# Performance work log

Hardware: AMD Instinct MI355X
Metric: run time of the kernel (lower is better)

## Reference

```python
import jax, jax.numpy as jnp
import numpy as np

N, E = 100000, 1600000
F_IN, H, K, C = 165, 128, 3, 2


def _norm_weights(edge_index, n):
    # PyG ChebConv.__norm__ with normalization='sym', lambda_max=2.0:
    # remove self loops, deg from row, w = -D^-1/2 A D^-1/2 off-diag, diag = 0.
    src, dst = edge_index[0], edge_index[1]
    mask = (src != dst).astype(jnp.float32)
    deg = jax.ops.segment_sum(mask, src, num_segments=n)
    dinv = jnp.where(deg > 0, jax.lax.rsqrt(jnp.where(deg > 0, deg, 1.0)), 0.0)
    return -dinv[src] * dinv[dst] * mask  # [E]


def _cheb_conv(x, W, b, src, dst, w, n):
    # Chebyshev recurrence: Tx0 = x, Tx1 = Lhat x, Tx_k = 2 Lhat Tx_{k-1} - Tx_{k-2}
    def prop(h):  # sparse Lhat @ h via gather + segment_sum
        return jax.ops.segment_sum(w[:, None] * h[src], dst, num_segments=n)

    out = x @ W[0]
    Tx0, Tx1 = x, prop(x)
    out = out + Tx1 @ W[1]
    for k in range(2, W.shape[0]):
        Tx2 = 2.0 * prop(Tx1) - Tx0
        out = out + Tx2 @ W[k]
        Tx0, Tx1 = Tx1, Tx2
    return out + b


def setup_inputs() -> dict:
    key = jax.random.key(0)
    ks = jax.random.split(key, 8)
    x = jax.random.normal(ks[0], (N, F_IN), dtype=jnp.float32)
    edge_index = jax.random.randint(ks[1], (2, E), 0, N, dtype=jnp.int64)
    s1 = 1.0 / np.sqrt(F_IN)
    s2 = 1.0 / np.sqrt(H)
    W1 = jax.random.uniform(ks[2], (K, F_IN, H), jnp.float32, -s1, s1)
    b1 = jnp.zeros((H,), jnp.float32)
    W2 = jax.random.uniform(ks[3], (K, H, H), jnp.float32, -s2, s2)
    b2 = jnp.zeros((H,), jnp.float32)
    Wl = jax.random.uniform(ks[4], (H, C), jnp.float32, -s2, s2)
    bl = jax.random.uniform(ks[5], (C,), jnp.float32, -s2, s2)
    return {"x": x, "edge_index": edge_index, "W1": W1, "b1": b1,
            "W2": W2, "b2": b2, "Wl": Wl, "bl": bl}


def reference(x, edge_index, W1, b1, W2, b2, Wl, bl):
    n = x.shape[0]
    src, dst = edge_index[0], edge_index[1]
    w = _norm_weights(edge_index, n)
    h = jax.nn.relu(_cheb_conv(x, W1, b1, src, dst, w, n))
    # F.dropout(training=self.training) is identity in eval mode
    h = h + _cheb_conv(h, W2, b2, src, dst, w, n)  # residual skip
    logits = jax.nn.log_softmax(h @ Wl + bl, axis=-1)
    return (logits, edge_index)
```

## Files before the change

kernel.cpp:

```cpp
#include <hip/hip_runtime.h>
#include <stdint.h>

typedef __bf16 bf16;
typedef unsigned char u8;
typedef __attribute__((ext_vector_type(8))) __bf16 bf16x8;
typedef __attribute__((ext_vector_type(4))) float f32x4;
typedef __attribute__((ext_vector_type(2))) float f32x2;

#define N_NODES 100000
#define F_IN 165
#define NB 391
#define NBLK 320

static inline int cdiv(int a, int b) { return (a + b - 1) / b; }

__device__ __forceinline__ float bfu(unsigned hw) {
  union { unsigned u; float f; } v; v.u = hw << 16; return v.f;
}
__device__ __forceinline__ unsigned packbf2(float a, float b) {
  bf16 x = (bf16)a, y = (bf16)b;
  unsigned short sx = __builtin_bit_cast(unsigned short, x);
  unsigned short sy = __builtin_bit_cast(unsigned short, y);
  return (unsigned)sx | ((unsigned)sy << 16);
}
__device__ __forceinline__ u8 f32_to_fp8(float v) {
  int t = __builtin_amdgcn_cvt_pk_fp8_f32(v, 0.f, 0, false);
  return (u8)(t & 0xff);
}

__device__ __forceinline__ void async16(const bf16* g, const bf16* l) {
  __builtin_amdgcn_global_load_lds(
      (const __attribute__((address_space(1))) void*)g,
      (__attribute__((address_space(3))) void*)l, 16, 0, 0);
}

__global__ void detect_k(const int* __restrict__ ei32, int* __restrict__ flag) {
  int i = blockIdx.x * 256 + threadIdx.x;
  int v = ei32[2 * i + 1];
  if (v != 0) atomicOr(flag, 1);
}


__global__ __launch_bounds__(256) void hist_k(const int* __restrict__ ei, int E,
                                              const int* __restrict__ flag,
                                              int* __restrict__ gcd, int* __restrict__ gcs) {
  __shared__ int hd[NB], hs[NB];
  int b = blockIdx.x, t = threadIdx.x;
  for (int i = t; i < NB; i += 256) { hd[i] = 0; hs[i] = 0; }
  __syncthreads();
  int sh = (*flag) ? 0 : 1;
  int CH = (E + NBLK - 1) / NBLK;
  int lo = b * CH, hi = min(E, lo + CH);
  for (int e = lo + t; e < hi; e += 256) {
    int s = ei[(size_t)e << sh];
    int d = ei[(size_t)(E + e) << sh];
    if ((unsigned)s < (unsigned)N_NODES && (unsigned)d < (unsigned)N_NODES && s != d) {
      atomicAdd(&hd[d >> 8], 1);
      atomicAdd(&hs[s >> 8], 1);
    }
  }
  __syncthreads();
  for (int i = t; i < NB; i += 256) {
    gcd[i * NBLK + b] = hd[i];
    gcs[i * NBLK + b] = hs[i];
  }
}

__global__ __launch_bounds__(256) void scat2_k(const int* __restrict__ ei, int E,
                                               const int* __restrict__ flag,
                                               const int* __restrict__ ofd,
                                               const int* __restrict__ ofs,
                                               unsigned* __restrict__ pkAll,
                                               float* __restrict__ eout) {
  __shared__ int based[NB], bases[NB];
  int b = blockIdx.x, t = threadIdx.x;
  for (int i = t; i < NB; i += 256) {
    based[i] = ofd[i * NBLK + b];
    bases[i] = ofs[i * NBLK + b];
  }
  __syncthreads();
  int sh = (*flag) ? 0 : 1;
  int CH = (E + NBLK - 1) / NBLK;
  int lo = b * CH, hi = min(E, lo + CH);
  for (int e = lo + t; e < hi; e += 256) {
    int s = ei[(size_t)e << sh];
    int d = ei[(size_t)(E + e) << sh];
    eout[e] = (float)s;
    eout[E + e] = (float)d;
    if ((unsigned)s < (unsigned)N_NODES && (unsigned)d < (unsigned)N_NODES && s != d) {
      int pd = atomicAdd(&based[d >> 8], 1);
      pkAll[pd] = ((unsigned)(d & 255) << 24) | (unsigned)s;
      int ps = atomicAdd(&bases[s >> 8], 1);
      pkAll[ps] = (unsigned)s;
    }
  }
}

__global__ __launch_bounds__(256) void fin_dst_k(const unsigned* __restrict__ pk,
                                                 const int* __restrict__ ofd,
                                                 const int* __restrict__ totald,
                                                 int* __restrict__ rowptr,
                                                 int* __restrict__ csr) {
  __shared__ int fh[256], fb[256];
  int b = blockIdx.x, t = threadIdx.x;
  int lo = ofd[b * NBLK];
  int hi = (b == NB - 1) ? *totald : ofd[(b + 1) * NBLK];
  fh[t] = 0;
  __syncthreads();
  for (int i = lo + t; i < hi; i += 256) atomicAdd(&fh[pk[i] >> 24], 1);
  __syncthreads();
  fb[t] = fh[t];
  __syncthreads();
  for (int offv = 1; offv < 256; offv <<= 1) {
    int x = (t >= offv) ? fb[t - offv] : 0;
    __syncthreads();
    fb[t] += x;
    __syncthreads();
  }
  int excl = fb[t] - fh[t];
  int node = b * 256 + t;
  if (node <= N_NODES) rowptr[node] = lo + excl;
  __syncthreads();
  fb[t] = lo + excl;
  __syncthreads();
  for (int i = lo + t; i < hi; i += 256) {
    unsigned v = pk[i];
    int pos = atomicAdd(&fb[v >> 24], 1);
    csr[pos] = (int)(v & 0xFFFFFFu);
  }
}

__global__ __launch_bounds__(256) void fin_src_k(const unsigned* __restrict__ pk,
                                                 const int* __restrict__ ofs,
                                                 const int* __restrict__ grand,
                                                 float* __restrict__ dinv) {
  __shared__ int fh[256];
  int b = blockIdx.x, t = threadIdx.x;
  int lo = ofs[b * NBLK];
  int hi = (b == NB - 1) ? *grand : ofs[(b + 1) * NBLK];
  fh[t] = 0;
  __syncthreads();
  for (int i = lo + t; i < hi; i += 256) atomicAdd(&fh[pk[i] & 255], 1);
  __syncthreads();
  int node = b * 256 + t;
  if (node < N_NODES) {
    int dg = fh[t];
    dinv[node] = dg > 0 ? rsqrtf((float)dg) : 0.f;
  }
}


__global__ void scanA_k(const int* __restrict__ cnt, int* __restrict__ bsum, int nElem) {
  __shared__ int s[256];
  int b = blockIdx.x, t = threadIdx.x;
  int base = b * 1024;
  int sum = 0;
  for (int i = t; i < 1024; i += 256) {
    int idx = base + i;
    sum += (idx < nElem) ? cnt[idx] : 0;
  }
  s[t] = sum; __syncthreads();
  for (int off = 128; off > 0; off >>= 1) {
    if (t < off) s[t] += s[t + off];
    __syncthreads();
  }
  if (t == 0) bsum[b] = s[0];
}

__global__ void scanB_k(int* __restrict__ bsum, int* __restrict__ totalOut, int nChunk) {
  __shared__ int s[256];
  int t = threadIdx.x;
  int v = (t < nChunk) ? bsum[t] : 0;
  s[t] = v; __syncthreads();
  for (int off = 1; off < 256; off <<= 1) {
    int x = (t >= off) ? s[t - off] : 0;
    __syncthreads();
    s[t] += x;
    __syncthreads();
  }
  int excl = s[t] - v;
  if (t < nChunk) bsum[t] = excl;
  if (t == 255) *totalOut = s[255];
}

__global__ void scanC_k(const int* __restrict__ cnt, const int* __restrict__ bsum,
                        int* __restrict__ outp, int nElem) {
  __shared__ int s[256];
  int b = blockIdx.x, t = threadIdx.x;
  int base = b * 1024 + t * 4;
  int v[4]; int tot = 0;
  for (int i = 0; i < 4; i++) {
    int idx = base + i;
    v[i] = (idx < nElem) ? cnt[idx] : 0;
    tot += v[i];
  }
  s[t] = tot; __syncthreads();
  for (int off = 1; off < 256; off <<= 1) {
    int x = (t >= off) ? s[t - off] : 0;
    __syncthreads();
    s[t] += x;
    __syncthreads();
  }
  int excl = s[t] - tot + bsum[b];
  for (int i = 0; i < 4; i++) {
    int idx = base + i;
    if (idx < nElem) { outp[idx] = excl; excl += v[i]; }
  }
}


__global__ void build_wct_k(const float* __restrict__ W, bf16* __restrict__ out, int Fin, int Kp) {
  int idx = blockIdx.x * 256 + threadIdx.x;
  if (idx >= 384 * Kp) return;
  int r = idx / Kp, k = idx % Kp;
  int t = r >> 7, j = r & 127;
  float v = 0.f;
  if (k < Fin) {
    if (t == 0)
      v = W[(size_t)k * 128 + j] - W[(size_t)2 * Fin * 128 + (size_t)k * 128 + j];
    else if (t == 1)
      v = W[(size_t)Fin * 128 + (size_t)k * 128 + j];
    else
      v = 2.f * W[(size_t)2 * Fin * 128 + (size_t)k * 128 + j];
  }
  out[(size_t)r * Kp + k] = (bf16)v;
}

__global__ void prep_k(const float* __restrict__ W2, const float* __restrict__ Wl,
                       const float* __restrict__ b2, const float* __restrict__ bl,
                       float* __restrict__ wlc, float* __restrict__ cc,
                       u8* __restrict__ g0, u8* __restrict__ g1) {
  int t = threadIdx.x;
  if (t < 16) ((unsigned*)(g0 + (size_t)N_NODES * 64))[t] = 0;
  else if (t < 32) ((unsigned*)(g1 + (size_t)N_NODES * 64))[t - 16] = 0;
  if (t < 128) {
    int f = t;
    float c00 = 0, c01 = 0, c10 = 0, c11 = 0, c20 = 0, c21 = 0;
    for (int k = 0; k < 128; k++) {
      float w0 = W2[(size_t)f * 128 + k];
      float w1 = W2[(size_t)128 * 128 + f * 128 + k];
      float w2 = W2[(size_t)2 * 128 * 128 + f * 128 + k];
      float l0 = Wl[k * 2], l1 = Wl[k * 2 + 1];
      c00 += (w0 - w2) * l0; c01 += (w0 - w2) * l1;
      c10 += w1 * l0;        c11 += w1 * l1;
      c20 += 2.f * w2 * l0;  c21 += 2.f * w2 * l1;
    }
    c00 += Wl[f * 2]; c01 += Wl[f * 2 + 1];
    wlc[0 * 128 + f] = c00; wlc[1 * 128 + f] = c01;
    wlc[2 * 128 + f] = c10; wlc[3 * 128 + f] = c11;
    wlc[4 * 128 + f] = c20; wlc[5 * 128 + f] = c21;
  } else if (t < 192) {
    int c = t - 128;
    float p0 = b2[2 * c] * Wl[(2 * c) * 2] + b2[2 * c + 1] * Wl[(2 * c + 1) * 2];
    float p1 = b2[2 * c] * Wl[(2 * c) * 2 + 1] + b2[2 * c + 1] * Wl[(2 * c + 1) * 2 + 1];
#pragma unroll
    for (int off = 32; off > 0; off >>= 1) {
      p0 += __shfl_down(p0, off);
      p1 += __shfl_down(p1, off);
    }
    if (c == 0) { cc[0] = p0 + bl[0]; cc[1] = p1 + bl[1]; }
  }
}

__global__ void pad_x_k(const float* __restrict__ x, bf16* __restrict__ xp) {
  int idx = blockIdx.x * 256 + threadIdx.x;
  if (idx >= N_NODES * 96) return;
  int n = idx / 96, k = (idx % 96) * 2;
  float a = (k < F_IN) ? x[(size_t)n * F_IN + k] : 0.f;
  float b = (k + 1 < F_IN) ? x[(size_t)n * F_IN + k + 1] : 0.f;
  *(unsigned*)(xp + (size_t)n * 192 + k) = packbf2(a, b);
}


__global__ __launch_bounds__(256) void gemm3_k(const bf16* __restrict__ A, int lda,
                                               const bf16* __restrict__ Bt, int K,
                                               bf16* __restrict__ C0, bf16* __restrict__ C1,
                                               u8* __restrict__ C2g,
                                               const float* __restrict__ dinv, int M) {
  __shared__ __align__(16) bf16 As[128 * 32];
  __shared__ __align__(16) bf16 Bs[128 * 32];
  const int b = blockIdx.x;
  const int xcd = b & 7, kk = b >> 3;
  const int y = kk % 3;
  const int m = xcd + 8 * (kk / 3);
  const int gmv = (M + 127) >> 7;
  if (m >= gmv) return;
  const int tid = threadIdx.x;
  const int w = tid >> 6, l = tid & 63;
  const int mBase = m * 128;
  const int nb = y * 128;
  const int wm = (w >> 1) * 64, wn = (w & 1) * 64;
  const int lr = l & 15, lq = l >> 4;
  f32x4 acc[4][4] = {};
  for (int k0 = 0; k0 < K; k0 += 32) {
#pragma unroll
    for (int p = 0; p < 2; ++p) {
      int q = w * 2 + p;
      int row = q * 16 + (l >> 2);
      int seg = (l & 3) * 8;
      int ar = mBase + row; if (ar > M - 1) ar = M - 1;
      async16(A + (size_t)ar * lda + k0 + seg, &As[q * 512]);
      async16(Bt + (size_t)(nb + row) * K + k0 + seg, &Bs[q * 512]);
    }
    __syncthreads();
    bf16x8 a[4], bb[4];
#pragma unroll
    for (int i = 0; i < 4; i++) a[i] = *(const bf16x8*)&As[(wm + i * 16 + lr) * 32 + lq * 8];
#pragma unroll
    for (int j = 0; j < 4; j++) bb[j] = *(const bf16x8*)&Bs[(wn + j * 16 + lr) * 32 + lq * 8];
#pragma unroll
    for (int i = 0; i < 4; i++)
#pragma unroll
      for (int j = 0; j < 4; j++)
        acc[i][j] = __builtin_amdgcn_mfma_f32_16x16x32_bf16(a[i], bb[j], acc[i][j], 0, 0, 0);
    __syncthreads();
  }
  if (y == 2) {
#pragma unroll
    for (int i = 0; i < 4; i++) {
#pragma unroll
      for (int r = 0; r < 4; r++) {
        int row = mBase + wm + i * 16 + lq * 4 + r;
        if (row < M) {
          float dv = dinv[row];
#pragma unroll
          for (int j = 0; j < 4; j++) {
            int col = wn + j * 16 + lr;
            C2g[(size_t)row * 128 + col] = f32_to_fp8(dv * acc[i][j][r]);
          }
        }
      }
    }
  } else {
    bf16* __restrict__ C = y ? C1 : C0;
#pragma unroll
    for (int i = 0; i < 4; i++) {
#pragma unroll
      for (int r = 0; r < 4; r++) {
        int row = mBase + wm + i * 16 + lq * 4 + r;
        if (row < M) {
#pragma unroll
          for (int j = 0; j < 4; j++) {
            int col = wn + j * 16 + lr;
            C[(size_t)row * 128 + col] = (bf16)acc[i][j][r];
          }
        }
      }
    }
  }
}

__global__ void cvt48_k(const u8* __restrict__ g8, u8* __restrict__ g4) {
  int i = blockIdx.x * 256 + threadIdx.x;
  if (i >= N_NODES * 16) return;
  int n = i >> 4, j = i & 15;
  uint2 w = *(const uint2*)(g8 + (size_t)n * 128 + j * 8);
  auto a0 = __builtin_amdgcn_cvt_pk_f32_fp8((int)w.x, false);
  auto a1 = __builtin_amdgcn_cvt_pk_f32_fp8((int)w.x, true);
  auto a2 = __builtin_amdgcn_cvt_pk_f32_fp8((int)w.y, false);
  auto a3 = __builtin_amdgcn_cvt_pk_f32_fp8((int)w.y, true);
  unsigned u = 0;
  u = __builtin_amdgcn_cvt_scalef32_pk_fp4_f32(u, 2.f * a0[0], 2.f * a0[1], 1.f, 0);
  u = __builtin_amdgcn_cvt_scalef32_pk_fp4_f32(u, 2.f * a1[0], 2.f * a1[1], 1.f, 1);
  u = __builtin_amdgcn_cvt_scalef32_pk_fp4_f32(u, 2.f * a2[0], 2.f * a2[1], 1.f, 2);
  u = __builtin_amdgcn_cvt_scalef32_pk_fp4_f32(u, 2.f * a3[0], 2.f * a3[1], 1.f, 3);
  *(unsigned*)(g4 + (size_t)n * 64 + j * 4) = u;
}

template <int MODE>
__global__ __launch_bounds__(256) void prop_k(const int* __restrict__ rowptr,
                                              const int* __restrict__ csr,
                                              const u8* __restrict__ g4,
                                              const float* __restrict__ dinv,
                                              const bf16* __restrict__ addA,
                                              const float* __restrict__ bias,
                                              const float* __restrict__ wlc,
                                              u8* __restrict__ out4,
                                              f32x2* __restrict__ V0,
                                              f32x2* __restrict__ V1,
                                              f32x2* __restrict__ V2s) {
  const int n = blockIdx.x * 4 + (threadIdx.x >> 6);
  const int lane = threadIdx.x & 63;
  const int qq = lane >> 4, j = lane & 15;
  const int beg = rowptr[n], end = rowptr[n + 1];
  const unsigned jb = (unsigned)j << 2;

  const float dn = dinv[n];
  uint4 ua = *(const uint4*)(addA + (size_t)n * 128 + j * 8);
  f32x4 bq0, bq1;
  if (MODE == 1) {
    bq0 = *(const f32x4*)(bias + 8 * j);
    bq1 = *(const f32x4*)(bias + 8 * j + 4);
  }

  f32x2 av[4] = {};

  int c[8];
#pragma unroll
  for (int u = 0; u < 8; u++) {
    int iu = beg + 4 * u + qq;
    c[u] = (iu < end) ? csr[iu] : N_NODES;
  }
  for (int e0 = beg; e0 < end; e0 += 32) {
    unsigned w[8];
#pragma unroll
    for (int u = 0; u < 8; u++)
      w[u] = *(const unsigned*)(g4 + (((unsigned)c[u] << 6) | jb));
#pragma unroll
    for (int u = 0; u < 8; u++) {
      int iu = e0 + 32 + 4 * u + qq;
      c[u] = (iu < end) ? csr[iu] : N_NODES;
    }
#pragma unroll
    for (int u = 0; u < 8; u++) {
      av[0] += __builtin_amdgcn_cvt_scalef32_pk_f32_fp4(w[u], 1.f, 0);
      av[1] += __builtin_amdgcn_cvt_scalef32_pk_f32_fp4(w[u], 1.f, 1);
      av[2] += __builtin_amdgcn_cvt_scalef32_pk_f32_fp4(w[u], 1.f, 2);
      av[3] += __builtin_amdgcn_cvt_scalef32_pk_f32_fp4(w[u], 1.f, 3);
    }
  }
#pragma unroll
  for (int off = 32; off >= 16; off >>= 1) {
#pragma unroll
    for (int k = 0; k < 4; k++) {
      av[k].x += __shfl_down(av[k].x, off);
      av[k].y += __shfl_down(av[k].y, off);
    }
  }

  f32x2 yv[4];
  yv[0].x = bfu(ua.x & 0xffffu); yv[0].y = bfu(ua.x >> 16);
  yv[1].x = bfu(ua.y & 0xffffu); yv[1].y = bfu(ua.y >> 16);
  yv[2].x = bfu(ua.z & 0xffffu); yv[2].y = bfu(ua.z >> 16);
  yv[3].x = bfu(ua.w & 0xffffu); yv[3].y = bfu(ua.w >> 16);

  if (MODE == 0) {
    if (qq == 0) {
      const float m1 = -dn * dn, m2 = 2.f * dn;
      f32x2 ov[4];
#pragma unroll
      for (int k = 0; k < 4; k++) ov[k] = av[k] * m1 + yv[k] * m2;
      unsigned u = 0;
      u = __builtin_amdgcn_cvt_scalef32_pk_fp4_f32(u, ov[0].x, ov[0].y, 1.f, 0);
      u = __builtin_amdgcn_cvt_scalef32_pk_fp4_f32(u, ov[1].x, ov[1].y, 1.f, 1);
      u = __builtin_amdgcn_cvt_scalef32_pk_fp4_f32(u, ov[2].x, ov[2].y, 1.f, 2);
      u = __builtin_amdgcn_cvt_scalef32_pk_fp4_f32(u, ov[3].x, ov[3].y, 1.f, 3);
      *(unsigned*)(out4 + (size_t)n * 64 + j * 4) = u;
    }
  } else {
    const float s = -0.5f * dn;
    f32x2 hv[4];
#pragma unroll
    for (int k = 0; k < 4; k++) {
      f32x2 t = av[k] * s + yv[k];
      f32x2 bb; bb.x = bq0[0], bb.y = bq0[1];
      if (k == 1) { bb.x = bq0[2]; bb.y = bq0[3]; }
      if (k == 2) { bb.x = bq1[0]; bb.y = bq1[1]; }
      if (k == 3) { bb.x = bq1[2]; bb.y = bq1[3]; }
      t += bb;
      hv[k].x = fmaxf(t.x, 0.f);
      hv[k].y = fmaxf(t.y, 0.f);
    }
    float p[6];
#pragma unroll
    for (int c2 = 0; c2 < 6; c2++) {
      f32x4 wa = *(const f32x4*)(wlc + c2 * 128 + 8 * j);
      f32x4 wb = *(const f32x4*)(wlc + c2 * 128 + 8 * j + 4);
      f32x2 w0; w0.x = wa[0]; w0.y = wa[1];
      f32x2 w1; w1.x = wa[2]; w1.y = wa[3];
      f32x2 w2; w2.x = wb[0]; w2.y = wb[1];
      f32x2 w3; w3.x = wb[2]; w3.y = wb[3];
      f32x2 acc = hv[0] * w0;
      acc += hv[1] * w1;
      acc += hv[2] * w2;
      acc += hv[3] * w3;
      p[c2] = acc.x + acc.y;
    }
#pragma unroll
    for (int off = 8; off >= 1; off >>= 1)
#pragma unroll
      for (int c2 = 0; c2 < 6; c2++) p[c2] += __shfl_down(p[c2], off);
    if (lane == 0) {
      f32x2 v0, v1, v2;
      v0.x = p[0]; v0.y = p[1];
      v1.x = p[2]; v1.y = p[3];
      v2.x = dn * p[4]; v2.y = dn * p[5];
      V0[n] = v0; V1[n] = v1; V2s[n] = v2;
    }
  }
}

template <int MODE>
__global__ __launch_bounds__(256) void propT_k(const int* __restrict__ rowptr,
                                               const int* __restrict__ csr,
                                               const f32x2* __restrict__ gsrc,
                                               const float* __restrict__ dinv,
                                               const f32x2* __restrict__ addv,
                                               const float* __restrict__ cc,
                                               f32x2* __restrict__ outv,
                                               float* __restrict__ fout) {
  int n = blockIdx.x * 16 + (threadIdx.x >> 4);
  int l = threadIdx.x & 15;
  int beg = rowptr[n], end = rowptr[n + 1];
  float s0 = 0.f, s1 = 0.f;
  for (int idx = beg + l; idx < end; idx += 16) {
    f32x2 v = gsrc[csr[idx]];
    s0 += v.x;
    s1 += v.y;
  }
#pragma unroll
  for (int off = 8; off > 0; off >>= 1) {
    s0 += __shfl_down(s0, off);
    s1 += __shfl_down(s1, off);
  }
  if (l != 0) return;
  float dn = dinv[n];
  f32x2 av = addv[n];
  if (MODE == 0) {
    f32x2 t;
    t.x = dn * (-dn * s0 + av.x);
    t.y = dn * (-dn * s1 + av.y);
    outv[n] = t;
  } else {
    float z0 = -dn * s0 + av.x + cc[0];
    float z1 = -dn * s1 + av.y + cc[1];
    float m = fmaxf(z0, z1);
    float lse = m + logf(expf(z0 - m) + expf(z1 - m));
    fout[(size_t)n * 2 + 0] = z0 - lse;
    fout[(size_t)n * 2 + 1] = z1 - lse;
  }
}


extern "C" void kernel_launch(void* const* d_in, const int* in_sizes, int n_in,
                              void* d_out, int out_size, void* d_ws, size_t ws_size,
                              hipStream_t stream) {
  const float* x = (const float*)d_in[0];
  const int* ei = (const int*)d_in[1];
  const float* W1 = (const float*)d_in[2];
  const float* b1 = (const float*)d_in[3];
  const float* W2 = (const float*)d_in[4];
  const float* b2 = (const float*)d_in[5];
  const float* Wl = (const float*)d_in[6];
  const float* bl = (const float*)d_in[7];
  float* outp = (float*)d_out;

  const int N = N_NODES;
  const int E = in_sizes[1] / 2;
  const int L = NB * NBLK;
  const int L2 = 2 * L;
  const int nChunkS = cdiv(L2, 1024);

  char* ws = (char*)d_ws;
  size_t off = 0;
  auto alloc = [&](size_t bytes) {
    off = (off + 255) & ~(size_t)255;
    size_t o = off;
    off += bytes;
    return o;
  };
  int* flag = (int*)(ws + alloc(4));
  int* gcAll = (int*)(ws + alloc((size_t)L2 * 4));
  int* bsum = (int*)(ws + alloc(1024));
  int* grand = (int*)(ws + alloc(4));
  int* rowptr = (int*)(ws + alloc((size_t)(N + 1) * 4));
  float* dinv = (float*)(ws + alloc((size_t)N * 4));
  unsigned* pkAll = (unsigned*)(ws + alloc((size_t)2 * E * 4));
  int* csr = (int*)(ws + alloc((size_t)E * 4));
  bf16* wct1 = (bf16*)(ws + alloc((size_t)384 * 192 * 2));
  float* wlc = (float*)(ws + alloc((size_t)128 * 6 * 4));
  float* cc = (float*)(ws + alloc(8));
  bf16* xp = (bf16*)(ws + alloc((size_t)N * 192 * 2));
  bf16* U0 = (bf16*)(ws + alloc((size_t)N * 128 * 2));
  bf16* U1 = (bf16*)(ws + alloc((size_t)N * 128 * 2));
  u8* G8 = (u8*)(ws + alloc((size_t)N * 128));
  u8* G0 = (u8*)(ws + alloc((size_t)(N + 1) * 64));
  u8* G1 = (u8*)(ws + alloc((size_t)(N + 1) * 64));
  f32x2* V0 = (f32x2*)(ws + alloc((size_t)N * 8));
  f32x2* V1 = (f32x2*)(ws + alloc((size_t)N * 8));
  f32x2* V2s = (f32x2*)(ws + alloc((size_t)N * 8));
  f32x2* tW = (f32x2*)(ws + alloc((size_t)N * 8));
  (void)ws_size;

  int* gcd = gcAll;
  int* gcs = gcAll + L;

  hipMemsetAsync(flag, 0, 4, stream);
  detect_k<<<256, 256, 0, stream>>>(ei, flag);

  hist_k<<<NBLK, 256, 0, stream>>>(ei, E, flag, gcd, gcs);
  scanA_k<<<nChunkS, 256, 0, stream>>>(gcAll, bsum, L2);
  scanB_k<<<1, 256, 0, stream>>>(bsum, grand, nChunkS);
  scanC_k<<<nChunkS, 256, 0, stream>>>(gcAll, bsum, gcAll, L2);
  scat2_k<<<NBLK, 256, 0, stream>>>(ei, E, flag, gcd, gcs, pkAll,
                                    outp + (size_t)2 * N);
  fin_dst_k<<<NB, 256, 0, stream>>>(pkAll, gcd, gcAll + L, rowptr, csr);
  fin_src_k<<<NB, 256, 0, stream>>>(pkAll, gcs, grand, dinv);

  prep_k<<<1, 256, 0, stream>>>(W2, Wl, b2, bl, wlc, cc, G0, G1);
  pad_x_k<<<cdiv(N * 96, 256), 256, 0, stream>>>(x, xp);
  build_wct_k<<<cdiv(384 * 192, 256), 256, 0, stream>>>(W1, wct1, F_IN, 192);

  const int gm = cdiv(N, 128);
  const int gmp = cdiv(gm, 8) * 8;
  gemm3_k<<<gmp * 3, 256, 0, stream>>>(xp, 192, wct1, 192, U0, U1, G8, dinv, N);
  cvt48_k<<<cdiv(N * 16, 256), 256, 0, stream>>>(G8, G0);
  prop_k<0><<<N / 4, 256, 0, stream>>>(rowptr, csr, G0, dinv, U1, nullptr, nullptr,
                                       G1, nullptr, nullptr, nullptr);
  prop_k<1><<<N / 4, 256, 0, stream>>>(rowptr, csr, G1, dinv, U0, b1, wlc,
                                       nullptr, V0, V1, V2s);
  propT_k<0><<<N / 16, 256, 0, stream>>>(rowptr, csr, V2s, dinv, V1, nullptr, tW, nullptr);
  propT_k<1><<<N / 16, 256, 0, stream>>>(rowptr, csr, tW, dinv, V0, cc, nullptr, outp);
}
```

Before: 403.5 us.

## Split fp4 propagation features into two 64-column halves for cache locality

Stores the fp4 gathered feature tables as two separate 32-byte-per-node arrays and runs each sparse propagation as two passes, one per feature half. Each pass gathers a smaller working set (3.2MB instead of 6.4MB), aiming for better L2/LLC hit rates on random neighbor gathers. Partial projection results of the first half are stored in a scratch buffer and combined in the second pass. This costs extra kernel launches, re-reading the CSR structure twice, and a round trip through the scratch buffer.

```diff
diff --git a/kernel.cpp b/kernel.cpp
--- a/kernel.cpp
+++ b/kernel.cpp
@@ -229,10 +229,13 @@
 __global__ void prep_k(const float* __restrict__ W2, const float* __restrict__ Wl,
                        const float* __restrict__ b2, const float* __restrict__ bl,
                        float* __restrict__ wlc, float* __restrict__ cc,
-                       u8* __restrict__ g0, u8* __restrict__ g1) {
+                       u8* __restrict__ g0a, u8* __restrict__ g0b,
+                       u8* __restrict__ g1a, u8* __restrict__ g1b) {
   int t = threadIdx.x;
-  if (t < 16) ((unsigned*)(g0 + (size_t)N_NODES * 64))[t] = 0;
-  else if (t < 32) ((unsigned*)(g1 + (size_t)N_NODES * 64))[t - 16] = 0;
+  if (t < 8) ((unsigned*)(g0a + (size_t)N_NODES * 32))[t] = 0;
+  else if (t < 16) ((unsigned*)(g0b + (size_t)N_NODES * 32))[t - 8] = 0;
+  else if (t < 24) ((unsigned*)(g1a + (size_t)N_NODES * 32))[t - 16] = 0;
+  else if (t < 32) ((unsigned*)(g1b + (size_t)N_NODES * 32))[t - 24] = 0;
   if (t < 128) {
     int f = t;
     float c00 = 0, c01 = 0, c10 = 0, c11 = 0, c20 = 0, c21 = 0;
@@ -350,7 +353,8 @@
   }
 }
 
-__global__ void cvt48_k(const u8* __restrict__ g8, u8* __restrict__ g4) {
+__global__ void cvt48_k(const u8* __restrict__ g8, u8* __restrict__ gA,
+                        u8* __restrict__ gB) {
   int i = blockIdx.x * 256 + threadIdx.x;
   if (i >= N_NODES * 16) return;
   int n = i >> 4, j = i & 15;
@@ -364,10 +368,12 @@
   u = __builtin_amdgcn_cvt_scalef32_pk_fp4_f32(u, 2.f * a1[0], 2.f * a1[1], 1.f, 1);
   u = __builtin_amdgcn_cvt_scalef32_pk_fp4_f32(u, 2.f * a2[0], 2.f * a2[1], 1.f, 2);
   u = __builtin_amdgcn_cvt_scalef32_pk_fp4_f32(u, 2.f * a3[0], 2.f * a3[1], 1.f, 3);
-  *(unsigned*)(g4 + (size_t)n * 64 + j * 4) = u;
-}
-
-template <int MODE>
+  u8* dst = (j < 8) ? (gA + (size_t)n * 32 + j * 4)
+                    : (gB + (size_t)n * 32 + (j - 8) * 4);
+  *(unsigned*)dst = u;
+}
+
+template <int MODE, int HALF>
 __global__ __launch_bounds__(256) void prop_k(const int* __restrict__ rowptr,
                                               const int* __restrict__ csr,
                                               const u8* __restrict__ g4,
@@ -378,41 +384,42 @@
                                               u8* __restrict__ out4,
                                               f32x2* __restrict__ V0,
                                               f32x2* __restrict__ V1,
-                                              f32x2* __restrict__ V2s) {
+                                              f32x2* __restrict__ V2s,
+                                              float* __restrict__ pbuf) {
   const int n = blockIdx.x * 4 + (threadIdx.x >> 6);
   const int lane = threadIdx.x & 63;
-  const int qq = lane >> 4, j = lane & 15;
+  const int o = lane >> 3, k = lane & 7;
   const int beg = rowptr[n], end = rowptr[n + 1];
-  const unsigned jb = (unsigned)j << 2;
+  const unsigned kb = (unsigned)k << 2;
 
   const float dn = dinv[n];
-  uint4 ua = *(const uint4*)(addA + (size_t)n * 128 + j * 8);
+  uint4 ua = *(const uint4*)((const u8*)addA + (size_t)n * 256 + HALF * 128 + k * 16);
   f32x4 bq0, bq1;
   if (MODE == 1) {
-    bq0 = *(const f32x4*)(bias + 8 * j);
-    bq1 = *(const f32x4*)(bias + 8 * j + 4);
+    bq0 = *(const f32x4*)(bias + HALF * 64 + 8 * k);
+    bq1 = *(const f32x4*)(bias + HALF * 64 + 8 * k + 4);
   }
 
   f32x2 av[4] = {};
 
-  int c[8];
-#pragma unroll
-  for (int u = 0; u < 8; u++) {
-    int iu = beg + 4 * u + qq;
+  int c[4];
+#pragma unroll
+  for (int u = 0; u < 4; u++) {
+    int iu = beg + 8 * u + o;
     c[u] = (iu < end) ? csr[iu] : N_NODES;
   }
   for (int e0 = beg; e0 < end; e0 += 32) {
-    unsigned w[8];
-#pragma unroll
-    for (int u = 0; u < 8; u++)
-      w[u] = *(const unsigned*)(g4 + (((unsigned)c[u] << 6) | jb));
-#pragma unroll
-    for (int u = 0; u < 8; u++) {
-      int iu = e0 + 32 + 4 * u + qq;
+    unsigned w[4];
+#pragma unroll
+    for (int u = 0; u < 4; u++)
+      w[u] = *(const unsigned*)(g4 + (((unsigned)c[u] << 5) | kb));
+#pragma unroll
+    for (int u = 0; u < 4; u++) {
+      int iu = e0 + 32 + 8 * u + o;
       c[u] = (iu < end) ? csr[iu] : N_NODES;
     }
 #pragma unroll
-    for (int u = 0; u < 8; u++) {
+    for (int u = 0; u < 4; u++) {
       av[0] += __builtin_amdgcn_cvt_scalef32_pk_f32_fp4(w[u], 1.f, 0);
       av[1] += __builtin_amdgcn_cvt_scalef32_pk_f32_fp4(w[u], 1.f, 1);
       av[2] += __builtin_amdgcn_cvt_scalef32_pk_f32_fp4(w[u], 1.f, 2);
@@ -420,11 +427,11 @@
     }
   }
 #pragma unroll
-  for (int off = 32; off >= 16; off >>= 1) {
-#pragma unroll
-    for (int k = 0; k < 4; k++) {
-      av[k].x += __shfl_down(av[k].x, off);
-      av[k].y += __shfl_down(av[k].y, off);
+  for (int off = 32; off >= 8; off >>= 1) {
+#pragma unroll
+    for (int m = 0; m < 4; m++) {
+      av[m].x += __shfl_down(av[m].x, off);
+      av[m].y += __shfl_down(av[m].y, off);
     }
   }
 
@@ -435,37 +442,37 @@
   yv[3].x = bfu(ua.w & 0xffffu); yv[3].y = bfu(ua.w >> 16);
 
   if (MODE == 0) {
-    if (qq == 0) {
+    if (lane < 8) {
       const float m1 = -dn * dn, m2 = 2.f * dn;
       f32x2 ov[4];
 #pragma unroll
-      for (int k = 0; k < 4; k++) ov[k] = av[k] * m1 + yv[k] * m2;
+      for (int m = 0; m < 4; m++) ov[m] = av[m] * m1 + yv[m] * m2;
       unsigned u = 0;
       u = __builtin_amdgcn_cvt_scalef32_pk_fp4_f32(u, ov[0].x, ov[0].y, 1.f, 0);
       u = __builtin_amdgcn_cvt_scalef32_pk_fp4_f32(u, ov[1].x, ov[1].y, 1.f, 1);
       u = __builtin_amdgcn_cvt_scalef32_pk_fp4_f32(u, ov[2].x, ov[2].y, 1.f, 2);
       u = __builtin_amdgcn_cvt_scalef32_pk_fp4_f32(u, ov[3].x, ov[3].y, 1.f, 3);
-      *(unsigned*)(out4 + (size_t)n * 64 + j * 4) = u;
+      *(unsigned*)(out4 + ((size_t)n << 5) + kb) = u;
     }
   } else {
     const float s = -0.5f * dn;
     f32x2 hv[4];
 #pragma unroll
-    for (int k = 0; k < 4; k++) {
-      f32x2 t = av[k] * s + yv[k];
+    for (int m = 0; m < 4; m++) {
+      f32x2 t = av[m] * s + yv[m];
       f32x2 bb; bb.x = bq0[0], bb.y = bq0[1];
-      if (k == 1) { bb.x = bq0[2]; bb.y = bq0[3]; }
-      if (k == 2) { bb.x = bq1[0]; bb.y = bq1[1]; }
-      if (k == 3) { bb.x = bq1[2]; bb.y = bq1[3]; }
+      if (m == 1) { bb.x = bq0[2]; bb.y = bq0[3]; }
+      if (m == 2) { bb.x = bq1[0]; bb.y = bq1[1]; }
+      if (m == 3) { bb.x = bq1[2]; bb.y = bq1[3]; }
       t += bb;
-      hv[k].x = fmaxf(t.x, 0.f);
-      hv[k].y = fmaxf(t.y, 0.f);
+      hv[m].x = fmaxf(t.x, 0.f);
+      hv[m].y = fmaxf(t.y, 0.f);
     }
     float p[6];
 #pragma unroll
     for (int c2 = 0; c2 < 6; c2++) {
-      f32x4 wa = *(const f32x4*)(wlc + c2 * 128 + 8 * j);
-      f32x4 wb = *(const f32x4*)(wlc + c2 * 128 + 8 * j + 4);
+      f32x4 wa = *(const f32x4*)(wlc + c2 * 128 + HALF * 64 + 8 * k);
+      f32x4 wb = *(const f32x4*)(wlc + c2 * 128 + HALF * 64 + 8 * k + 4);
       f32x2 w0; w0.x = wa[0]; w0.y = wa[1];
       f32x2 w1; w1.x = wa[2]; w1.y = wa[3];
       f32x2 w2; w2.x = wb[0]; w2.y = wb[1];
@@ -477,15 +484,29 @@
       p[c2] = acc.x + acc.y;
     }
 #pragma unroll
-    for (int off = 8; off >= 1; off >>= 1)
+    for (int off = 4; off >= 1; off >>= 1)
 #pragma unroll
       for (int c2 = 0; c2 < 6; c2++) p[c2] += __shfl_down(p[c2], off);
     if (lane == 0) {
-      f32x2 v0, v1, v2;
-      v0.x = p[0]; v0.y = p[1];
-      v1.x = p[2]; v1.y = p[3];
-      v2.x = dn * p[4]; v2.y = dn * p[5];
-      V0[n] = v0; V1[n] = v1; V2s[n] = v2;
+      float* pb = pbuf + (size_t)n * 6;
+      if (HALF == 0) {
+        f32x2 q0, q1, q2;
+        q0.x = p[0]; q0.y = p[1];
+        q1.x = p[2]; q1.y = p[3];
+        q2.x = p[4]; q2.y = p[5];
+        *(f32x2*)(pb + 0) = q0;
+        *(f32x2*)(pb + 2) = q1;
+        *(f32x2*)(pb + 4) = q2;
+      } else {
+        f32x2 q0 = *(const f32x2*)(pb + 0);
+        f32x2 q1 = *(const f32x2*)(pb + 2);
+        f32x2 q2 = *(const f32x2*)(pb + 4);
+        f32x2 v0, v1, v2;
+        v0.x = p[0] + q0.x; v0.y = p[1] + q0.y;
+        v1.x = p[2] + q1.x; v1.y = p[3] + q1.y;
+        v2.x = dn * (p[4] + q2.x); v2.y = dn * (p[5] + q2.y);
+        V0[n] = v0; V1[n] = v1; V2s[n] = v2;
+      }
     }
   }
 }
@@ -574,8 +595,11 @@
   bf16* U0 = (bf16*)(ws + alloc((size_t)N * 128 * 2));
   bf16* U1 = (bf16*)(ws + alloc((size_t)N * 128 * 2));
   u8* G8 = (u8*)(ws + alloc((size_t)N * 128));
-  u8* G0 = (u8*)(ws + alloc((size_t)(N + 1) * 64));
-  u8* G1 = (u8*)(ws + alloc((size_t)(N + 1) * 64));
+  u8* G0A = (u8*)(ws + alloc((size_t)(N + 1) * 32));
+  u8* G0B = (u8*)(ws + alloc((size_t)(N + 1) * 32));
+  u8* G1A = (u8*)(ws + alloc((size_t)(N + 1) * 32));
+  u8* G1B = (u8*)(ws + alloc((size_t)(N + 1) * 32));
+  float* pbuf = (float*)(ws + alloc((size_t)N * 6 * 4));
   f32x2* V0 = (f32x2*)(ws + alloc((size_t)N * 8));
   f32x2* V1 = (f32x2*)(ws + alloc((size_t)N * 8));
   f32x2* V2s = (f32x2*)(ws + alloc((size_t)N * 8));
@@ -597,18 +621,25 @@
   fin_dst_k<<<NB, 256, 0, stream>>>(pkAll, gcd, gcAll + L, rowptr, csr);
   fin_src_k<<<NB, 256, 0, stream>>>(pkAll, gcs, grand, dinv);
 
-  prep_k<<<1, 256, 0, stream>>>(W2, Wl, b2, bl, wlc, cc, G0, G1);
+  prep_k<<<1, 256, 0, stream>>>(W2, Wl, b2, bl, wlc, cc, G0A, G0B, G1A, G1B);
   pad_x_k<<<cdiv(N * 96, 256), 256, 0, stream>>>(x, xp);
   build_wct_k<<<cdiv(384 * 192, 256), 256, 0, stream>>>(W1, wct1, F_IN, 192);
 
   const int gm = cdiv(N, 128);
   const int gmp = cdiv(gm, 8) * 8;
   gemm3_k<<<gmp * 3, 256, 0, stream>>>(xp, 192, wct1, 192, U0, U1, G8, dinv, N);
-  cvt48_k<<<cdiv(N * 16, 256), 256, 0, stream>>>(G8, G0);
-  prop_k<0><<<N / 4, 256, 0, stream>>>(rowptr, csr, G0, dinv, U1, nullptr, nullptr,
-                                       G1, nullptr, nullptr, nullptr);
-  prop_k<1><<<N / 4, 256, 0, stream>>>(rowptr, csr, G1, dinv, U0, b1, wlc,
-                                       nullptr, V0, V1, V2s);
+  cvt48_k<<<cdiv(N * 16, 256), 256, 0, stream>>>(G8, G0A, G0B);
+  prop_k<0, 0><<<N / 4, 256, 0, stream>>>(rowptr, csr, G0A, dinv, U1, nullptr,
+                                          nullptr, G1A, nullptr, nullptr,
+                                          nullptr, nullptr);
+  prop_k<0, 1><<<N / 4, 256, 0, stream>>>(rowptr, csr, G0B, dinv, U1, nullptr,
+                                          nullptr, G1B, nullptr, nullptr,
+                                          nullptr, nullptr);
+  prop_k<1, 0><<<N / 4, 256, 0, stream>>>(rowptr, csr, G1A, dinv, U0, b1, wlc,
+                                          nullptr, nullptr, nullptr, nullptr,
+                                          pbuf);
+  prop_k<1, 1><<<N / 4, 256, 0, stream>>>(rowptr, csr, G1B, dinv, U0, b1, wlc,
+                                          nullptr, V0, V1, V2s, pbuf);
   propT_k<0><<<N / 16, 256, 0, stream>>>(rowptr, csr, V2s, dinv, V1, nullptr, tW, nullptr);
   propT_k<1><<<N / 16, 256, 0, stream>>>(rowptr, csr, tW, dinv, V0, cc, nullptr, outp);
 }
```

New measurement: 482.5 us. 19.6% more time.
